# Performance work log

Hardware: AMD Instinct MI355X
Metric: run time of the kernel (lower is better)

The kernel has to match this reference:

```python
import jax, jax.numpy as jnp
import numpy as np

EPS = 1e-8

def _gelu(x):
    return jax.nn.gelu(x, approximate=False)  # torch F.gelu default (erf)

def _film_pool(feat, q, film_w, film_b, hid_w, hid_b, fin_w, fin_b):
    # feat: (B,C,H,W), q: (B,Q,E)
    B, C, H, W = feat.shape
    f = feat.reshape(B, C, H * W).transpose(0, 2, 1)            # (B,HW,C)
    gb = q @ film_w + film_b                                    # (B,Q,2C)
    gamma, beta = jnp.split(gb, 2, axis=-1)                     # (B,Q,C) each
    mod = gamma[:, :, None, :] * f[:, None, :, :] + beta[:, :, None, :]  # (B,Q,HW,C)
    h = _gelu(mod @ hid_w + hid_b)                              # (B,Q,HW,Hh)
    attn = jax.nn.sigmoid(h @ fin_w + fin_b)                    # (B,Q,HW,1)
    pooled = (attn * mod).sum(axis=2) / (attn.sum(axis=2) + EPS)  # (B,Q,C)
    return pooled, attn[..., 0]                                 # attn map (B,Q,HW)

def setup_inputs() -> dict:
    key = jax.random.key(0)
    ks = jax.random.split(key, 32)
    B, Q, E, Hh = 2, 32, 768, 128
    chans = [64, 128, 256]
    hws = [(80, 80), (40, 40), (20, 20)]
    d = {}
    d['feat0'] = jax.random.normal(ks[0], (B, chans[0], *hws[0]), jnp.float32)
    d['feat1'] = jax.random.normal(ks[1], (B, chans[1], *hws[1]), jnp.float32)
    d['feat2'] = jax.random.normal(ks[2], (B, chans[2], *hws[2]), jnp.float32)
    d['fact_embeddings'] = jax.random.normal(ks[3], (B, Q, E), jnp.float32)
    for i, C in enumerate(chans):
        d[f'film_w{i}'] = jax.random.normal(ks[4 + 4 * i], (E, 2 * C), jnp.float32) * 0.02
        d[f'film_b{i}'] = jnp.zeros((2 * C,), jnp.float32)
        d[f'hid_w{i}'] = jax.random.normal(ks[5 + 4 * i], (C, Hh), jnp.float32) * 0.05
        d[f'hid_b{i}'] = jnp.zeros((Hh,), jnp.float32)
        d[f'fin_w{i}'] = jax.random.normal(ks[6 + 4 * i], (Hh, 1), jnp.float32) * 0.05
        d[f'fin_b{i}'] = jnp.zeros((1,), jnp.float32)
    in_dim = sum(chans) + hws[-1][0] * hws[-1][1]  # 448 + 400 = 848
    d['mlp_w1'] = jax.random.normal(ks[20], (in_dim, 512), jnp.float32) * 0.02
    d['mlp_b1'] = jnp.zeros((512,), jnp.float32)
    d['mlp_w2'] = jax.random.normal(ks[21], (512, 256), jnp.float32) * 0.02
    d['mlp_b2'] = jnp.zeros((256,), jnp.float32)
    d['mlp_w3'] = jax.random.normal(ks[22], (256, 1), jnp.float32) * 0.02
    d['mlp_b3'] = jnp.zeros((1,), jnp.float32)
    return d

def reference(feat0, feat1, feat2, fact_embeddings,
              film_w0, film_b0, hid_w0, hid_b0, fin_w0, fin_b0,
              film_w1, film_b1, hid_w1, hid_b1, fin_w1, fin_b1,
              film_w2, film_b2, hid_w2, hid_b2, fin_w2, fin_b2,
              mlp_w1, mlp_b1, mlp_w2, mlp_b2, mlp_w3, mlp_b3):
    q = fact_embeddings
    p0, _ = _film_pool(feat0, q, film_w0, film_b0, hid_w0, hid_b0, fin_w0, fin_b0)
    p1, _ = _film_pool(feat1, q, film_w1, film_b1, hid_w1, hid_b1, fin_w1, fin_b1)
    p2, a2 = _film_pool(feat2, q, film_w2, film_b2, hid_w2, hid_b2, fin_w2, fin_b2)
    cat = jnp.concatenate([p0, p1, p2, a2], axis=2)  # (B,Q,848)
    x = _gelu(cat @ mlp_w1 + mlp_b1)
    x = _gelu(x @ mlp_w2 + mlp_b2)
    logits = (x @ mlp_w3 + mlp_b3)[..., 0]  # (B,Q)
    return logits
```

## Files before the change

kernel.cpp:

```cpp
#include <hip/hip_runtime.h>
#include <math.h>

#define BQ 64
#define HH 128
#define EPS 1e-8f

typedef short bf16x8 __attribute__((ext_vector_type(8)));
typedef float f32x4  __attribute__((ext_vector_type(4)));

__device__ __forceinline__ float gelu_exact(float x) {
    return 0.5f * x * (1.0f + erff(x * 0.70710678118654752440f));
}

__device__ __forceinline__ unsigned bf16_rne(float x) {
    unsigned u = __float_as_uint(x);
    return (u + 0x7FFFu + ((u >> 16) & 1u)) >> 16;
}
__device__ __forceinline__ uint2 split_pack(float a, float b) {
    unsigned ha = bf16_rne(a);
    float fa = __uint_as_float(ha << 16);
    unsigned la = bf16_rne(a - fa);
    unsigned hb = bf16_rne(b);
    float fb = __uint_as_float(hb << 16);
    unsigned lb = bf16_rne(b - fb);
    uint2 r; r.x = ha | (hb << 16); r.y = la | (lb << 16);
    return r;
}

__global__ __launch_bounds__(256)
void film2_kernel(const float* __restrict__ qe,
                  const float* __restrict__ fw0, const float* __restrict__ fb0,
                  const float* __restrict__ fw1, const float* __restrict__ fb1,
                  const float* __restrict__ fw2, const float* __restrict__ fb2,
                  float* __restrict__ gb0, float* __restrict__ gb1, float* __restrict__ gb2)
{
    __shared__ float sq[768];
    __shared__ float sP[256];
    const int tid = threadIdx.x, bq = blockIdx.x, chunk = blockIdx.y;
    int s, o0;
    if (chunk == 0)      { s = 0; o0 = 0; }
    else if (chunk <= 2) { s = 1; o0 = (chunk - 1) * 128; }
    else                 { s = 2; o0 = (chunk - 3) * 128; }
    const float* fw  = s == 0 ? fw0 : s == 1 ? fw1 : fw2;
    const float* fbv = s == 0 ? fb0 : s == 1 ? fb1 : fb2;
    float* gb        = s == 0 ? gb0 : s == 1 ? gb1 : gb2;
    const int twoC = 128 << s;

    for (int i = tid; i < 768; i += 256) sq[i] = qe[bq * 768 + i];
    __syncthreads();

    const int o = o0 + (tid & 127), half = tid >> 7;
    const int e0 = half * 384;
    float a0 = 0.f, a1 = 0.f;
    #pragma unroll 2
    for (int e = 0; e < 384; e += 2) {
        a0 = fmaf(sq[e0 + e],     fw[(e0 + e) * twoC + o],     a0);
        a1 = fmaf(sq[e0 + e + 1], fw[(e0 + e + 1) * twoC + o], a1);
    }
    sP[tid] = a0 + a1;
    __syncthreads();
    if (tid < 128) {
        int oo = o0 + tid;
        gb[bq * twoC + oo] = sP[tid] + sP[tid + 128] + fbv[oo];
    }
}

__global__ __launch_bounds__(256)
void b2_kernel(const float* __restrict__ gb0, const float* __restrict__ gb1,
               const float* __restrict__ gb2,
               const float* __restrict__ hw0_, const float* __restrict__ hb0,
               const float* __restrict__ hw1_, const float* __restrict__ hb1,
               const float* __restrict__ hw2_, const float* __restrict__ hb2,
               float* __restrict__ b20, float* __restrict__ b21, float* __restrict__ b22)
{
    __shared__ float sBeta[256];
    __shared__ float sP[256];
    const int tid = threadIdx.x, bq = blockIdx.x, s = blockIdx.y;
    const float* gb = s == 0 ? gb0 : s == 1 ? gb1 : gb2;
    const float* hw = s == 0 ? hw0_ : s == 1 ? hw1_ : hw2_;
    const float* hb = s == 0 ? hb0 : s == 1 ? hb1 : hb2;
    float* b2       = s == 0 ? b20 : s == 1 ? b21 : b22;
    const int C = 64 << s;

    for (int i = tid; i < C; i += 256) sBeta[i] = gb[bq * 2 * C + C + i];
    __syncthreads();
    const int j = tid & 127, half = tid >> 7;
    const int c0 = half * (C / 2);
    float acc = 0.f;
    for (int c = 0; c < C / 2; ++c)
        acc = fmaf(sBeta[c0 + c], hw[(c0 + c) * HH + j], acc);
    sP[tid] = acc;
    __syncthreads();
    if (tid < 128) b2[bq * HH + tid] = hb[tid] + sP[tid] + sP[tid + 128];
}

__global__ __launch_bounds__(256)
void pack_feat_kernel(const float* __restrict__ f0, const float* __restrict__ f1,
                      const float* __restrict__ f2,
                      unsigned short* __restrict__ p0h, unsigned short* __restrict__ p0l,
                      unsigned short* __restrict__ p1h, unsigned short* __restrict__ p1l,
                      unsigned short* __restrict__ p2h, unsigned short* __restrict__ p2l)
{
    int i = blockIdx.x * 256 + threadIdx.x;
    const float* f; unsigned short *oh, *ol; int HW; int idx;
    if (i < 102400)      { f = f0; oh = p0h; ol = p0l; HW = 6400; idx = i; }
    else if (i < 153600) { f = f1; oh = p1h; ol = p1l; HW = 1600; idx = i - 102400; }
    else if (i < 179200) { f = f2; oh = p2h; ol = p2l; HW = 400;  idx = i - 153600; }
    else return;
    const int px = idx % HW;
    const int cgb = idx / HW;
    const float* src = f + ((size_t)cgb * 8) * HW + px;
    float a[8];
    #pragma unroll
    for (int k = 0; k < 8; ++k) a[k] = src[(size_t)k * HW];
    unsigned hwd[4], lwd[4];
    #pragma unroll
    for (int k = 0; k < 4; ++k) {
        uint2 p = split_pack(a[2 * k], a[2 * k + 1]);
        hwd[k] = p.x; lwd[k] = p.y;
    }
    *(uint4*)&oh[(size_t)idx * 8] = make_uint4(hwd[0], hwd[1], hwd[2], hwd[3]);
    *(uint4*)&ol[(size_t)idx * 8] = make_uint4(lwd[0], lwd[1], lwd[2], lwd[3]);
}

__global__ __launch_bounds__(256)
void pack_gw_kernel(const float* __restrict__ gb0, const float* __restrict__ gb1,
                    const float* __restrict__ gb2,
                    const float* __restrict__ hw0_, const float* __restrict__ hw1_,
                    const float* __restrict__ hw2_,
                    unsigned short* __restrict__ g0h, unsigned short* __restrict__ g0l,
                    unsigned short* __restrict__ g1h, unsigned short* __restrict__ g1l,
                    unsigned short* __restrict__ g2h, unsigned short* __restrict__ g2l)
{
    int i = blockIdx.x * 256 + threadIdx.x;
    const float *gb, *hw; unsigned short *oh, *ol; int C, idx;
    if (i < 65536)       { gb = gb0; hw = hw0_; oh = g0h; ol = g0l; C = 64;  idx = i; }
    else if (i < 196608) { gb = gb1; hw = hw1_; oh = g1h; ol = g1l; C = 128; idx = i - 65536; }
    else if (i < 458752) { gb = gb2; hw = hw2_; oh = g2h; ol = g2l; C = 256; idx = i - 196608; }
    else return;
    const int j  = idx & 127;
    const int cg = (idx >> 7) % (C / 8);
    const int bq = idx / (128 * (C / 8));
    const int c0 = cg * 8;
    const float* g = gb + bq * 2 * C;
    float a[8];
    #pragma unroll
    for (int k = 0; k < 8; ++k) a[k] = g[c0 + k] * hw[(size_t)(c0 + k) * HH + j];
    unsigned hwd[4], lwd[4];
    #pragma unroll
    for (int k = 0; k < 4; ++k) {
        uint2 p = split_pack(a[2 * k], a[2 * k + 1]);
        hwd[k] = p.x; lwd[k] = p.y;
    }
    *(uint4*)&oh[(size_t)idx * 8] = make_uint4(hwd[0], hwd[1], hwd[2], hwd[3]);
    *(uint4*)&ol[(size_t)idx * 8] = make_uint4(lwd[0], lwd[1], lwd[2], lwd[3]);
}

template<int C, bool WRITE_ATTN>
__device__ __forceinline__
void pool_body(const float* __restrict__ feat, int HW,
               const unsigned short* __restrict__ fh, const unsigned short* __restrict__ fl,
               const unsigned short* __restrict__ gwh, const unsigned short* __restrict__ gwl,
               const float* __restrict__ b2, const float* __restrict__ finw,
               const float* __restrict__ finb,
               float* __restrict__ Sout, float* __restrict__ attn_out,
               int bq, int tile,
               unsigned short* sB, float* sAttn)
{
    const int tid  = threadIdx.x;
    const int w    = tid >> 6;
    const int lane = tid & 63;
    const int l15  = lane & 15, l4 = lane >> 4;
    const int b    = bq >> 5;
    const int px0  = tile * 256;
    constexpr int CG = C / 8;
    const float* fbase = feat + (size_t)b * C * HW;

    f32x4 acc[2][8];
    #pragma unroll
    for (int jt = 0; jt < 8; ++jt) {
        float bv = b2[bq * HH + jt * 16 + l15];
        acc[0][jt] = (f32x4){bv, bv, bv, bv};
        acc[1][jt] = (f32x4){bv, bv, bv, bv};
    }

    const int apx0 = min(px0 + (w * 2 + 0) * 16 + l15, HW - 1);
    const int apx1 = min(px0 + (w * 2 + 1) * 16 + l15, HW - 1);
    const unsigned short* fhp = fh + (size_t)b * CG * HW * 8;
    const unsigned short* flp = fl + (size_t)b * CG * HW * 8;
    const unsigned short* gbh = gwh + (size_t)bq * CG * 128 * 8;
    const unsigned short* gbl = gwl + (size_t)bq * CG * 128 * 8;

    for (int ks = 0; ks < CG / 4; ++ks) {
        const size_t arow = (size_t)(ks * 4 + l4) * HW;
        const bf16x8 Ahi0 = *(const bf16x8*)(fhp + (arow + apx0) * 8);
        const bf16x8 Alo0 = *(const bf16x8*)(flp + (arow + apx0) * 8);
        const bf16x8 Ahi1 = *(const bf16x8*)(fhp + (arow + apx1) * 8);
        const bf16x8 Alo1 = *(const bf16x8*)(flp + (arow + apx1) * 8);

        {
            const uint4* srcH = (const uint4*)(gbh + (size_t)ks * 4096);
            const uint4* srcL = (const uint4*)(gbl + (size_t)ks * 4096);
            uint4* dst = (uint4*)sB;
            dst[tid]       = srcH[tid];
            dst[512 + tid] = srcL[tid];
        }
        __syncthreads();

        const int bofs = (l4 * 128 + l15) * 8;
        #pragma unroll
        for (int jt = 0; jt < 8; ++jt) {
            const bf16x8 Bhi = *(const bf16x8*)(sB + bofs + jt * 128);
            const bf16x8 Blo = *(const bf16x8*)(sB + 4096 + bofs + jt * 128);
            acc[0][jt] = __builtin_amdgcn_mfma_f32_16x16x32_bf16(Alo0, Bhi, acc[0][jt], 0, 0, 0);
            acc[0][jt] = __builtin_amdgcn_mfma_f32_16x16x32_bf16(Ahi0, Blo, acc[0][jt], 0, 0, 0);
            acc[0][jt] = __builtin_amdgcn_mfma_f32_16x16x32_bf16(Ahi0, Bhi, acc[0][jt], 0, 0, 0);
            acc[1][jt] = __builtin_amdgcn_mfma_f32_16x16x32_bf16(Alo1, Bhi, acc[1][jt], 0, 0, 0);
            acc[1][jt] = __builtin_amdgcn_mfma_f32_16x16x32_bf16(Ahi1, Blo, acc[1][jt], 0, 0, 0);
            acc[1][jt] = __builtin_amdgcn_mfma_f32_16x16x32_bf16(Ahi1, Bhi, acc[1][jt], 0, 0, 0);
        }
        __syncthreads();
    }

    const float fb0 = finb[0];
    #pragma unroll
    for (int p = 0; p < 2; ++p) {
        float pl[4] = {0.f, 0.f, 0.f, 0.f};
        #pragma unroll
        for (int jt = 0; jt < 8; ++jt) {
            float fw = finw[jt * 16 + l15];
            #pragma unroll
            for (int r = 0; r < 4; ++r)
                pl[r] = fmaf(gelu_exact(acc[p][jt][r]), fw, pl[r]);
        }
        #pragma unroll
        for (int r = 0; r < 4; ++r) {
            pl[r] += __shfl_xor(pl[r], 1);
            pl[r] += __shfl_xor(pl[r], 2);
            pl[r] += __shfl_xor(pl[r], 4);
            pl[r] += __shfl_xor(pl[r], 8);
        }
        if (l15 == 0) {
            #pragma unroll
            for (int r = 0; r < 4; ++r) {
                int lpx = (w * 2 + p) * 16 + l4 * 4 + r;
                int px  = px0 + lpx;
                float a = (px < HW) ? 1.0f / (1.0f + expf(-(pl[r] + fb0))) : 0.0f;
                sAttn[lpx] = a;
                if (WRITE_ATTN && px < HW) attn_out[bq * HW + px] = a;
            }
        }
    }
    __syncthreads();

    if (tid < 256) {
        float sa = sAttn[tid];
        #pragma unroll
        for (int d = 1; d < 64; d <<= 1) sa += __shfl_xor(sa, d);
        if (lane == 0) atomicAdd(&Sout[bq * (C + 1) + C], sa);
    }

    constexpr int CPW = C / 8;
    #pragma unroll 1
    for (int ci = 0; ci < CPW; ++ci) {
        const int c2 = w * CPW + ci;
        const float* fr = fbase + (size_t)c2 * HW;
        float s = 0.f;
        #pragma unroll
        for (int k = 0; k < 4; ++k) {
            int lpx = lane + 64 * k;
            int gc = min(px0 + lpx, HW - 1);
            s = fmaf(fr[gc], sAttn[lpx], s);
        }
        #pragma unroll
        for (int d = 1; d < 64; d <<= 1) s += __shfl_xor(s, d);
        if (lane == 0) atomicAdd(&Sout[bq * (C + 1) + c2], s);
    }
}

__global__ __launch_bounds__(512)
void pool_fused(const float* __restrict__ feat0, const float* __restrict__ feat1,
                const float* __restrict__ feat2,
                const unsigned short* __restrict__ f0h, const unsigned short* __restrict__ f0l,
                const unsigned short* __restrict__ f1h, const unsigned short* __restrict__ f1l,
                const unsigned short* __restrict__ f2h, const unsigned short* __restrict__ f2l,
                const unsigned short* __restrict__ g0h, const unsigned short* __restrict__ g0l,
                const unsigned short* __restrict__ g1h, const unsigned short* __restrict__ g1l,
                const unsigned short* __restrict__ g2h, const unsigned short* __restrict__ g2l,
                const float* __restrict__ b20, const float* __restrict__ b21,
                const float* __restrict__ b22,
                const float* __restrict__ finw0, const float* __restrict__ finb0,
                const float* __restrict__ finw1, const float* __restrict__ finb1,
                const float* __restrict__ finw2, const float* __restrict__ finb2,
                float* __restrict__ S0, float* __restrict__ S1, float* __restrict__ S2,
                float* __restrict__ attn2)
{
    __shared__ __align__(16) unsigned short sB[8192];
    __shared__ float sAttn[256];
    const int blk = blockIdx.x;
    if (blk < 128) {
        int bq = blk >> 1, t = blk & 1;
        pool_body<256, true>(feat2, 400, f2h, f2l, g2h, g2l, b22, finw2, finb2,
                             S2, attn2, bq, t, sB, sAttn);
    } else if (blk < 576) {
        int bb = blk - 128; int bq = bb / 7, t = bb % 7;
        pool_body<128, false>(feat1, 1600, f1h, f1l, g1h, g1l, b21, finw1, finb1,
                              S1, nullptr, bq, t, sB, sAttn);
    } else {
        int bb = blk - 576; int bq = bb / 25, t = bb % 25;
        pool_body<64, false>(feat0, 6400, f0h, f0l, g0h, g0l, b20, finw0, finb0,
                             S0, nullptr, bq, t, sB, sAttn);
    }
}

__global__ __launch_bounds__(256)
void mlp1_kernel(const float* __restrict__ S0, const float* __restrict__ S1,
                 const float* __restrict__ S2,
                 const float* __restrict__ gb0, const float* __restrict__ gb1,
                 const float* __restrict__ gb2,
                 const float* __restrict__ attn2,
                 const float* __restrict__ w1, const float* __restrict__ b1,
                 float* __restrict__ X1)
{
    __shared__ float sCat[848];
    __shared__ float sP[256];
    const int tid = threadIdx.x, bq = blockIdx.x;

    for (int i = tid; i < 448; i += 256) {
        int sc, c;
        if (i < 64)       { sc = 0; c = i; }
        else if (i < 192) { sc = 1; c = i - 64; }
        else              { sc = 2; c = i - 192; }
        const int C = 64 << sc;
        const float* So = (sc == 0) ? S0 : (sc == 1) ? S1 : S2;
        const float* g  = (sc == 0) ? gb0 : (sc == 1) ? gb1 : gb2;
        float Sa = So[bq * (C + 1) + C];
        float Sf = So[bq * (C + 1) + c];
        float gamma = g[bq * 2 * C + c];
        float beta  = g[bq * 2 * C + C + c];
        sCat[i] = (gamma * Sf + beta * Sa) / (Sa + EPS);
    }
    for (int i = tid; i < 400; i += 256) sCat[448 + i] = attn2[bq * 400 + i];
    __syncthreads();

    const int o = blockIdx.y * 128 + (tid & 127), half = tid >> 7;
    const int k0 = half * 424;
    float a0 = 0.f, a1 = 0.f;
    #pragma unroll 2
    for (int k = 0; k < 424; k += 2) {
        a0 = fmaf(sCat[k0 + k],     w1[(k0 + k) * 512 + o],     a0);
        a1 = fmaf(sCat[k0 + k + 1], w1[(k0 + k + 1) * 512 + o], a1);
    }
    sP[tid] = a0 + a1;
    __syncthreads();
    if (tid < 128) {
        int oo = blockIdx.y * 128 + tid;
        X1[bq * 512 + oo] = sP[tid] + sP[tid + 128] + b1[oo];
    }
}

__global__ __launch_bounds__(256)
void mlp23_kernel(const float* __restrict__ X1,
                  const float* __restrict__ w2, const float* __restrict__ b2,
                  const float* __restrict__ w3, const float* __restrict__ b3,
                  float* __restrict__ out)
{
    __shared__ float sX1[512];
    __shared__ float sX2[256];
    __shared__ float sR[4];
    const int tid = threadIdx.x, bq = blockIdx.x;
    for (int i = tid; i < 512; i += 256) sX1[i] = gelu_exact(X1[bq * 512 + i]);
    __syncthreads();
    float a0 = b2[tid], a1 = 0.f, a2 = 0.f, a3 = 0.f;
    #pragma unroll 4
    for (int k = 0; k < 512; k += 4) {
        a0 = fmaf(sX1[k],     w2[(k)     * 256 + tid], a0);
        a1 = fmaf(sX1[k + 1], w2[(k + 1) * 256 + tid], a1);
        a2 = fmaf(sX1[k + 2], w2[(k + 2) * 256 + tid], a2);
        a3 = fmaf(sX1[k + 3], w2[(k + 3) * 256 + tid], a3);
    }
    sX2[tid] = gelu_exact((a0 + a1) + (a2 + a3));
    __syncthreads();
    float p = sX2[tid] * w3[tid];
    #pragma unroll
    for (int d = 1; d < 64; d <<= 1) p += __shfl_xor(p, d);
    if ((tid & 63) == 0) sR[tid >> 6] = p;
    __syncthreads();
    if (tid == 0) out[bq] = sR[0] + sR[1] + sR[2] + sR[3] + b3[0];
}

extern "C" void kernel_launch(void* const* d_in, const int* in_sizes, int n_in,
                              void* d_out, int out_size, void* d_ws, size_t ws_size,
                              hipStream_t stream)
{
    const float* feat0 = (const float*)d_in[0];
    const float* feat1 = (const float*)d_in[1];
    const float* feat2 = (const float*)d_in[2];
    const float* qe    = (const float*)d_in[3];
    const float* film_w0 = (const float*)d_in[4];
    const float* film_b0 = (const float*)d_in[5];
    const float* hid_w0  = (const float*)d_in[6];
    const float* hid_b0  = (const float*)d_in[7];
    const float* fin_w0  = (const float*)d_in[8];
    const float* fin_b0  = (const float*)d_in[9];
    const float* film_w1 = (const float*)d_in[10];
    const float* film_b1 = (const float*)d_in[11];
    const float* hid_w1  = (const float*)d_in[12];
    const float* hid_b1  = (const float*)d_in[13];
    const float* fin_w1  = (const float*)d_in[14];
    const float* fin_b1  = (const float*)d_in[15];
    const float* film_w2 = (const float*)d_in[16];
    const float* film_b2 = (const float*)d_in[17];
    const float* hid_w2  = (const float*)d_in[18];
    const float* hid_b2  = (const float*)d_in[19];
    const float* fin_w2  = (const float*)d_in[20];
    const float* fin_b2  = (const float*)d_in[21];
    const float* mlp_w1  = (const float*)d_in[22];
    const float* mlp_b1  = (const float*)d_in[23];
    const float* mlp_w2  = (const float*)d_in[24];
    const float* mlp_b2  = (const float*)d_in[25];
    const float* mlp_w3  = (const float*)d_in[26];
    const float* mlp_b3  = (const float*)d_in[27];

    float* ws = (float*)d_ws;
    float* S0    = ws;
    float* S1    = ws + 4160;
    float* S2    = ws + 12416;
    float* gb0   = ws + 28864;
    float* gb1   = ws + 37056;
    float* gb2   = ws + 53440;
    float* b20   = ws + 86208;
    float* b21   = ws + 94400;
    float* b22   = ws + 102592;
    float* attn2 = ws + 110784;
    float* X1    = ws + 136384;

    unsigned short* us = (unsigned short*)(ws + 169216);
    unsigned short* f0h = us;
    unsigned short* f0l = f0h + 819200;
    unsigned short* f1h = f0l + 819200;
    unsigned short* f1l = f1h + 409600;
    unsigned short* f2h = f1l + 409600;
    unsigned short* f2l = f2h + 204800;
    unsigned short* g0h = f2l + 204800;
    unsigned short* g0l = g0h + 524288;
    unsigned short* g1h = g0l + 524288;
    unsigned short* g1l = g1h + 1048576;
    unsigned short* g2h = g1l + 1048576;
    unsigned short* g2l = g2h + 2097152;

    hipMemsetAsync(d_ws, 0, 28864 * sizeof(float), stream);

    pack_feat_kernel<<<700, 256, 0, stream>>>(
        feat0, feat1, feat2, f0h, f0l, f1h, f1l, f2h, f2l);

    film2_kernel<<<dim3(BQ, 7), 256, 0, stream>>>(
        qe, film_w0, film_b0, film_w1, film_b1, film_w2, film_b2,
        gb0, gb1, gb2);

    pack_gw_kernel<<<1792, 256, 0, stream>>>(
        gb0, gb1, gb2, hid_w0, hid_w1, hid_w2,
        g0h, g0l, g1h, g1l, g2h, g2l);

    b2_kernel<<<dim3(BQ, 3), 256, 0, stream>>>(
        gb0, gb1, gb2,
        hid_w0, hid_b0, hid_w1, hid_b1, hid_w2, hid_b2,
        b20, b21, b22);

    pool_fused<<<2176, 512, 0, stream>>>(
        feat0, feat1, feat2,
        f0h, f0l, f1h, f1l, f2h, f2l,
        g0h, g0l, g1h, g1l, g2h, g2l,
        b20, b21, b22,
        fin_w0, fin_b0, fin_w1, fin_b1, fin_w2, fin_b2,
        S0, S1, S2, attn2);

    mlp1_kernel<<<dim3(BQ, 4), 256, 0, stream>>>(
        S0, S1, S2, gb0, gb1, gb2, attn2, mlp_w1, mlp_b1, X1);

    mlp23_kernel<<<BQ, 256, 0, stream>>>(
        X1, mlp_w2, mlp_b2, mlp_w3, mlp_b3, (float*)d_out);
}
```

Before: 258.0 us.

## Process two queries per pool block and merge prep kernels into two launches

```diff
diff --git a/kernel.cpp b/kernel.cpp
--- a/kernel.cpp
+++ b/kernel.cpp
@@ -27,81 +27,14 @@
     return r;
 }
 
-__global__ __launch_bounds__(256)
-void film2_kernel(const float* __restrict__ qe,
-                  const float* __restrict__ fw0, const float* __restrict__ fb0,
-                  const float* __restrict__ fw1, const float* __restrict__ fb1,
-                  const float* __restrict__ fw2, const float* __restrict__ fb2,
-                  float* __restrict__ gb0, float* __restrict__ gb1, float* __restrict__ gb2)
-{
-    __shared__ float sq[768];
-    __shared__ float sP[256];
-    const int tid = threadIdx.x, bq = blockIdx.x, chunk = blockIdx.y;
-    int s, o0;
-    if (chunk == 0)      { s = 0; o0 = 0; }
-    else if (chunk <= 2) { s = 1; o0 = (chunk - 1) * 128; }
-    else                 { s = 2; o0 = (chunk - 3) * 128; }
-    const float* fw  = s == 0 ? fw0 : s == 1 ? fw1 : fw2;
-    const float* fbv = s == 0 ? fb0 : s == 1 ? fb1 : fb2;
-    float* gb        = s == 0 ? gb0 : s == 1 ? gb1 : gb2;
-    const int twoC = 128 << s;
-
-    for (int i = tid; i < 768; i += 256) sq[i] = qe[bq * 768 + i];
-    __syncthreads();
-
-    const int o = o0 + (tid & 127), half = tid >> 7;
-    const int e0 = half * 384;
-    float a0 = 0.f, a1 = 0.f;
-    #pragma unroll 2
-    for (int e = 0; e < 384; e += 2) {
-        a0 = fmaf(sq[e0 + e],     fw[(e0 + e) * twoC + o],     a0);
-        a1 = fmaf(sq[e0 + e + 1], fw[(e0 + e + 1) * twoC + o], a1);
-    }
-    sP[tid] = a0 + a1;
-    __syncthreads();
-    if (tid < 128) {
-        int oo = o0 + tid;
-        gb[bq * twoC + oo] = sP[tid] + sP[tid + 128] + fbv[oo];
-    }
-}
-
-__global__ __launch_bounds__(256)
-void b2_kernel(const float* __restrict__ gb0, const float* __restrict__ gb1,
-               const float* __restrict__ gb2,
-               const float* __restrict__ hw0_, const float* __restrict__ hb0,
-               const float* __restrict__ hw1_, const float* __restrict__ hb1,
-               const float* __restrict__ hw2_, const float* __restrict__ hb2,
-               float* __restrict__ b20, float* __restrict__ b21, float* __restrict__ b22)
-{
-    __shared__ float sBeta[256];
-    __shared__ float sP[256];
-    const int tid = threadIdx.x, bq = blockIdx.x, s = blockIdx.y;
-    const float* gb = s == 0 ? gb0 : s == 1 ? gb1 : gb2;
-    const float* hw = s == 0 ? hw0_ : s == 1 ? hw1_ : hw2_;
-    const float* hb = s == 0 ? hb0 : s == 1 ? hb1 : hb2;
-    float* b2       = s == 0 ? b20 : s == 1 ? b21 : b22;
-    const int C = 64 << s;
-
-    for (int i = tid; i < C; i += 256) sBeta[i] = gb[bq * 2 * C + C + i];
-    __syncthreads();
-    const int j = tid & 127, half = tid >> 7;
-    const int c0 = half * (C / 2);
-    float acc = 0.f;
-    for (int c = 0; c < C / 2; ++c)
-        acc = fmaf(sBeta[c0 + c], hw[(c0 + c) * HH + j], acc);
-    sP[tid] = acc;
-    __syncthreads();
-    if (tid < 128) b2[bq * HH + tid] = hb[tid] + sP[tid] + sP[tid + 128];
-}
-
-__global__ __launch_bounds__(256)
-void pack_feat_kernel(const float* __restrict__ f0, const float* __restrict__ f1,
-                      const float* __restrict__ f2,
-                      unsigned short* __restrict__ p0h, unsigned short* __restrict__ p0l,
-                      unsigned short* __restrict__ p1h, unsigned short* __restrict__ p1l,
-                      unsigned short* __restrict__ p2h, unsigned short* __restrict__ p2l)
-{
-    int i = blockIdx.x * 256 + threadIdx.x;
+__device__ __forceinline__
+void pack_feat_body(int i,
+                    const float* __restrict__ f0, const float* __restrict__ f1,
+                    const float* __restrict__ f2,
+                    unsigned short* __restrict__ p0h, unsigned short* __restrict__ p0l,
+                    unsigned short* __restrict__ p1h, unsigned short* __restrict__ p1l,
+                    unsigned short* __restrict__ p2h, unsigned short* __restrict__ p2l)
+{
     const float* f; unsigned short *oh, *ol; int HW; int idx;
     if (i < 102400)      { f = f0; oh = p0h; ol = p0l; HW = 6400; idx = i; }
     else if (i < 153600) { f = f1; oh = p1h; ol = p1l; HW = 1600; idx = i - 102400; }
@@ -124,37 +57,115 @@
 }
 
 __global__ __launch_bounds__(256)
-void pack_gw_kernel(const float* __restrict__ gb0, const float* __restrict__ gb1,
-                    const float* __restrict__ gb2,
-                    const float* __restrict__ hw0_, const float* __restrict__ hw1_,
-                    const float* __restrict__ hw2_,
-                    unsigned short* __restrict__ g0h, unsigned short* __restrict__ g0l,
-                    unsigned short* __restrict__ g1h, unsigned short* __restrict__ g1l,
-                    unsigned short* __restrict__ g2h, unsigned short* __restrict__ g2l)
-{
-    int i = blockIdx.x * 256 + threadIdx.x;
-    const float *gb, *hw; unsigned short *oh, *ol; int C, idx;
-    if (i < 65536)       { gb = gb0; hw = hw0_; oh = g0h; ol = g0l; C = 64;  idx = i; }
-    else if (i < 196608) { gb = gb1; hw = hw1_; oh = g1h; ol = g1l; C = 128; idx = i - 65536; }
-    else if (i < 458752) { gb = gb2; hw = hw2_; oh = g2h; ol = g2l; C = 256; idx = i - 196608; }
-    else return;
-    const int j  = idx & 127;
-    const int cg = (idx >> 7) % (C / 8);
-    const int bq = idx / (128 * (C / 8));
-    const int c0 = cg * 8;
-    const float* g = gb + bq * 2 * C;
-    float a[8];
-    #pragma unroll
-    for (int k = 0; k < 8; ++k) a[k] = g[c0 + k] * hw[(size_t)(c0 + k) * HH + j];
-    unsigned hwd[4], lwd[4];
-    #pragma unroll
-    for (int k = 0; k < 4; ++k) {
-        uint2 p = split_pack(a[2 * k], a[2 * k + 1]);
-        hwd[k] = p.x; lwd[k] = p.y;
-    }
-    *(uint4*)&oh[(size_t)idx * 8] = make_uint4(hwd[0], hwd[1], hwd[2], hwd[3]);
-    *(uint4*)&ol[(size_t)idx * 8] = make_uint4(lwd[0], lwd[1], lwd[2], lwd[3]);
-}
+void prep1_kernel(const float* __restrict__ f0, const float* __restrict__ f1,
+                  const float* __restrict__ f2,
+                  unsigned short* __restrict__ p0h, unsigned short* __restrict__ p0l,
+                  unsigned short* __restrict__ p1h, unsigned short* __restrict__ p1l,
+                  unsigned short* __restrict__ p2h, unsigned short* __restrict__ p2l,
+                  const float* __restrict__ qe,
+                  const float* __restrict__ fw0, const float* __restrict__ fb0,
+                  const float* __restrict__ fw1, const float* __restrict__ fb1,
+                  const float* __restrict__ fw2, const float* __restrict__ fb2,
+                  float* __restrict__ gb0, float* __restrict__ gb1, float* __restrict__ gb2)
+{
+    const int tid = threadIdx.x;
+    if (blockIdx.x < 700) {
+        pack_feat_body(blockIdx.x * 256 + tid, f0, f1, f2, p0h, p0l, p1h, p1l, p2h, p2l);
+        return;
+    }
+    __shared__ float sq[768];
+    __shared__ float sP[256];
+    const int bb = blockIdx.x - 700;
+    const int chunk = bb >> 6, bq = bb & 63;
+    int s, o0;
+    if (chunk == 0)      { s = 0; o0 = 0; }
+    else if (chunk <= 2) { s = 1; o0 = (chunk - 1) * 128; }
+    else                 { s = 2; o0 = (chunk - 3) * 128; }
+    const float* fw  = s == 0 ? fw0 : s == 1 ? fw1 : fw2;
+    const float* fbv = s == 0 ? fb0 : s == 1 ? fb1 : fb2;
+    float* gb        = s == 0 ? gb0 : s == 1 ? gb1 : gb2;
+    const int twoC = 128 << s;
+
+    for (int i = tid; i < 768; i += 256) sq[i] = qe[bq * 768 + i];
+    __syncthreads();
+    const int o = o0 + (tid & 127), half = tid >> 7;
+    const int e0 = half * 384;
+    float a0 = 0.f, a1 = 0.f;
+    #pragma unroll 2
+    for (int e = 0; e < 384; e += 2) {
+        a0 = fmaf(sq[e0 + e],     fw[(e0 + e) * twoC + o],     a0);
+        a1 = fmaf(sq[e0 + e + 1], fw[(e0 + e + 1) * twoC + o], a1);
+    }
+    sP[tid] = a0 + a1;
+    __syncthreads();
+    if (tid < 128) {
+        int oo = o0 + tid;
+        gb[bq * twoC + oo] = sP[tid] + sP[tid + 128] + fbv[oo];
+    }
+}
+
+__global__ __launch_bounds__(256)
+void prep2_kernel(const float* __restrict__ gb0, const float* __restrict__ gb1,
+                  const float* __restrict__ gb2,
+                  const float* __restrict__ hw0_, const float* __restrict__ hb0,
+                  const float* __restrict__ hw1_, const float* __restrict__ hb1,
+                  const float* __restrict__ hw2_, const float* __restrict__ hb2,
+                  unsigned short* __restrict__ g0h, unsigned short* __restrict__ g0l,
+                  unsigned short* __restrict__ g1h, unsigned short* __restrict__ g1l,
+                  unsigned short* __restrict__ g2h, unsigned short* __restrict__ g2l,
+                  float* __restrict__ b20, float* __restrict__ b21, float* __restrict__ b22)
+{
+    const int tid = threadIdx.x;
+    if (blockIdx.x < 1792) {
+        int i = blockIdx.x * 256 + tid;
+        const float *gb, *hw; unsigned short *oh, *ol; int C, idx;
+        if (i < 65536)       { gb = gb0; hw = hw0_; oh = g0h; ol = g0l; C = 64;  idx = i; }
+        else if (i < 196608) { gb = gb1; hw = hw1_; oh = g1h; ol = g1l; C = 128; idx = i - 65536; }
+        else                 { gb = gb2; hw = hw2_; oh = g2h; ol = g2l; C = 256; idx = i - 196608; }
+        const int j  = idx & 127;
+        const int cg = (idx >> 7) % (C / 8);
+        const int bq = idx / (128 * (C / 8));
+        const int c0 = cg * 8;
+        const float* g = gb + bq * 2 * C;
+        float a[8];
+        #pragma unroll
+        for (int k = 0; k < 8; ++k) a[k] = g[c0 + k] * hw[(size_t)(c0 + k) * HH + j];
+        unsigned hwd[4], lwd[4];
+        #pragma unroll
+        for (int k = 0; k < 4; ++k) {
+            uint2 p = split_pack(a[2 * k], a[2 * k + 1]);
+            hwd[k] = p.x; lwd[k] = p.y;
+        }
+        *(uint4*)&oh[(size_t)idx * 8] = make_uint4(hwd[0], hwd[1], hwd[2], hwd[3]);
+        *(uint4*)&ol[(size_t)idx * 8] = make_uint4(lwd[0], lwd[1], lwd[2], lwd[3]);
+        return;
+    }
+    __shared__ float sBeta[256];
+    __shared__ float sP[256];
+    const int bb = blockIdx.x - 1792;
+    const int s = bb >> 6, bq = bb & 63;
+    const float* gb = s == 0 ? gb0 : s == 1 ? gb1 : gb2;
+    const float* hw = s == 0 ? hw0_ : s == 1 ? hw1_ : hw2_;
+    const float* hb = s == 0 ? hb0 : s == 1 ? hb1 : hb2;
+    float* b2       = s == 0 ? b20 : s == 1 ? b21 : b22;
+    const int C = 64 << s;
+
+    for (int i = tid; i < C; i += 256) sBeta[i] = gb[bq * 2 * C + C + i];
+    __syncthreads();
+    const int j = tid & 127, half = tid >> 7;
+    const int c0 = half * (C / 2);
+    float acc = 0.f;
+    for (int c = 0; c < C / 2; ++c)
+        acc = fmaf(sBeta[c0 + c], hw[(c0 + c) * HH + j], acc);
+    sP[tid] = acc;
+    __syncthreads();
+    if (tid < 128) b2[bq * HH + tid] = hb[tid] + sP[tid] + sP[tid + 128];
+}
+
+#define MFMA3(ACC, ALO, AHI, BH, BL)                                            \
+    ACC = __builtin_amdgcn_mfma_f32_16x16x32_bf16(ALO, BH, ACC, 0, 0, 0);       \
+    ACC = __builtin_amdgcn_mfma_f32_16x16x32_bf16(AHI, BL, ACC, 0, 0, 0);       \
+    ACC = __builtin_amdgcn_mfma_f32_16x16x32_bf16(AHI, BH, ACC, 0, 0, 0);
 
 template<int C, bool WRITE_ATTN>
 __device__ __forceinline__
@@ -164,32 +175,38 @@
                const float* __restrict__ b2, const float* __restrict__ finw,
                const float* __restrict__ finb,
                float* __restrict__ Sout, float* __restrict__ attn_out,
-               int bq, int tile,
+               int b, int qp, int tile,
                unsigned short* sB, float* sAttn)
 {
     const int tid  = threadIdx.x;
     const int w    = tid >> 6;
     const int lane = tid & 63;
     const int l15  = lane & 15, l4 = lane >> 4;
-    const int b    = bq >> 5;
     const int px0  = tile * 256;
     constexpr int CG = C / 8;
+    const int bq0 = b * 32 + qp * 2;
+    const int bq1 = bq0 + 1;
     const float* fbase = feat + (size_t)b * C * HW;
 
-    f32x4 acc[2][8];
+    f32x4 accA[2][8], accB[2][8];
     #pragma unroll
     for (int jt = 0; jt < 8; ++jt) {
-        float bv = b2[bq * HH + jt * 16 + l15];
-        acc[0][jt] = (f32x4){bv, bv, bv, bv};
-        acc[1][jt] = (f32x4){bv, bv, bv, bv};
+        float bv0 = b2[bq0 * HH + jt * 16 + l15];
+        float bv1 = b2[bq1 * HH + jt * 16 + l15];
+        accA[0][jt] = (f32x4){bv0, bv0, bv0, bv0};
+        accA[1][jt] = (f32x4){bv0, bv0, bv0, bv0};
+        accB[0][jt] = (f32x4){bv1, bv1, bv1, bv1};
+        accB[1][jt] = (f32x4){bv1, bv1, bv1, bv1};
     }
 
     const int apx0 = min(px0 + (w * 2 + 0) * 16 + l15, HW - 1);
     const int apx1 = min(px0 + (w * 2 + 1) * 16 + l15, HW - 1);
     const unsigned short* fhp = fh + (size_t)b * CG * HW * 8;
     const unsigned short* flp = fl + (size_t)b * CG * HW * 8;
-    const unsigned short* gbh = gwh + (size_t)bq * CG * 128 * 8;
-    const unsigned short* gbl = gwl + (size_t)bq * CG * 128 * 8;
+    const unsigned short* q0h = gwh + (size_t)bq0 * CG * 128 * 8;
+    const unsigned short* q0l = gwl + (size_t)bq0 * CG * 128 * 8;
+    const unsigned short* q1h = gwh + (size_t)bq1 * CG * 128 * 8;
+    const unsigned short* q1l = gwl + (size_t)bq1 * CG * 128 * 8;
 
     for (int ks = 0; ks < CG / 4; ++ks) {
         const size_t arow = (size_t)(ks * 4 + l4) * HW;
@@ -197,67 +214,76 @@
         const bf16x8 Alo0 = *(const bf16x8*)(flp + (arow + apx0) * 8);
         const bf16x8 Ahi1 = *(const bf16x8*)(fhp + (arow + apx1) * 8);
         const bf16x8 Alo1 = *(const bf16x8*)(flp + (arow + apx1) * 8);
-
         {
-            const uint4* srcH = (const uint4*)(gbh + (size_t)ks * 4096);
-            const uint4* srcL = (const uint4*)(gbl + (size_t)ks * 4096);
             uint4* dst = (uint4*)sB;
-            dst[tid]       = srcH[tid];
-            dst[512 + tid] = srcL[tid];
+            dst[tid]        = ((const uint4*)(q0h + (size_t)ks * 4096))[tid];
+            dst[512  + tid] = ((const uint4*)(q0l + (size_t)ks * 4096))[tid];
+            dst[1024 + tid] = ((const uint4*)(q1h + (size_t)ks * 4096))[tid];
+            dst[1536 + tid] = ((const uint4*)(q1l + (size_t)ks * 4096))[tid];
         }
         __syncthreads();
-
         const int bofs = (l4 * 128 + l15) * 8;
         #pragma unroll
         for (int jt = 0; jt < 8; ++jt) {
-            const bf16x8 Bhi = *(const bf16x8*)(sB + bofs + jt * 128);
-            const bf16x8 Blo = *(const bf16x8*)(sB + 4096 + bofs + jt * 128);
-            acc[0][jt] = __builtin_amdgcn_mfma_f32_16x16x32_bf16(Alo0, Bhi, acc[0][jt], 0, 0, 0);
-            acc[0][jt] = __builtin_amdgcn_mfma_f32_16x16x32_bf16(Ahi0, Blo, acc[0][jt], 0, 0, 0);
-            acc[0][jt] = __builtin_amdgcn_mfma_f32_16x16x32_bf16(Ahi0, Bhi, acc[0][jt], 0, 0, 0);
-            acc[1][jt] = __builtin_amdgcn_mfma_f32_16x16x32_bf16(Alo1, Bhi, acc[1][jt], 0, 0, 0);
-            acc[1][jt] = __builtin_amdgcn_mfma_f32_16x16x32_bf16(Ahi1, Blo, acc[1][jt], 0, 0, 0);
-            acc[1][jt] = __builtin_amdgcn_mfma_f32_16x16x32_bf16(Ahi1, Bhi, acc[1][jt], 0, 0, 0);
+            const bf16x8 B0h = *(const bf16x8*)(sB + bofs + jt * 128);
+            const bf16x8 B0l = *(const bf16x8*)(sB + 4096 + bofs + jt * 128);
+            MFMA3(accA[0][jt], Alo0, Ahi0, B0h, B0l)
+            MFMA3(accA[1][jt], Alo1, Ahi1, B0h, B0l)
+            const bf16x8 B1h = *(const bf16x8*)(sB + 8192 + bofs + jt * 128);
+            const bf16x8 B1l = *(const bf16x8*)(sB + 12288 + bofs + jt * 128);
+            MFMA3(accB[0][jt], Alo0, Ahi0, B1h, B1l)
+            MFMA3(accB[1][jt], Alo1, Ahi1, B1h, B1l)
         }
         __syncthreads();
     }
 
     const float fb0 = finb[0];
     #pragma unroll
-    for (int p = 0; p < 2; ++p) {
-        float pl[4] = {0.f, 0.f, 0.f, 0.f};
+    for (int pt = 0; pt < 2; ++pt) {
+        float p0[4] = {0.f, 0.f, 0.f, 0.f};
+        float p1[4] = {0.f, 0.f, 0.f, 0.f};
         #pragma unroll
         for (int jt = 0; jt < 8; ++jt) {
-            float fw = finw[jt * 16 + l15];
+            float fwv = finw[jt * 16 + l15];
             #pragma unroll
-            for (int r = 0; r < 4; ++r)
-                pl[r] = fmaf(gelu_exact(acc[p][jt][r]), fw, pl[r]);
+            for (int r = 0; r < 4; ++r) {
+                p0[r] = fmaf(gelu_exact(accA[pt][jt][r]), fwv, p0[r]);
+                p1[r] = fmaf(gelu_exact(accB[pt][jt][r]), fwv, p1[r]);
+            }
         }
         #pragma unroll
         for (int r = 0; r < 4; ++r) {
-            pl[r] += __shfl_xor(pl[r], 1);
-            pl[r] += __shfl_xor(pl[r], 2);
-            pl[r] += __shfl_xor(pl[r], 4);
-            pl[r] += __shfl_xor(pl[r], 8);
+            p0[r] += __shfl_xor(p0[r], 1);  p1[r] += __shfl_xor(p1[r], 1);
+            p0[r] += __shfl_xor(p0[r], 2);  p1[r] += __shfl_xor(p1[r], 2);
+            p0[r] += __shfl_xor(p0[r], 4);  p1[r] += __shfl_xor(p1[r], 4);
+            p0[r] += __shfl_xor(p0[r], 8);  p1[r] += __shfl_xor(p1[r], 8);
         }
         if (l15 == 0) {
             #pragma unroll
             for (int r = 0; r < 4; ++r) {
-                int lpx = (w * 2 + p) * 16 + l4 * 4 + r;
+                int lpx = (w * 2 + pt) * 16 + l4 * 4 + r;
                 int px  = px0 + lpx;
-                float a = (px < HW) ? 1.0f / (1.0f + expf(-(pl[r] + fb0))) : 0.0f;
-                sAttn[lpx] = a;
-                if (WRITE_ATTN && px < HW) attn_out[bq * HW + px] = a;
+                float a0v = (px < HW) ? 1.0f / (1.0f + expf(-(p0[r] + fb0))) : 0.0f;
+                float a1v = (px < HW) ? 1.0f / (1.0f + expf(-(p1[r] + fb0))) : 0.0f;
+                sAttn[lpx]       = a0v;
+                sAttn[256 + lpx] = a1v;
+                if (WRITE_ATTN && px < HW) {
+                    attn_out[bq0 * HW + px] = a0v;
+                    attn_out[bq1 * HW + px] = a1v;
+                }
             }
         }
     }
     __syncthreads();
 
-    if (tid < 256) {
+    {
         float sa = sAttn[tid];
         #pragma unroll
         for (int d = 1; d < 64; d <<= 1) sa += __shfl_xor(sa, d);
-        if (lane == 0) atomicAdd(&Sout[bq * (C + 1) + C], sa);
+        if (lane == 0) {
+            int bqx = (tid < 256) ? bq0 : bq1;
+            atomicAdd(&Sout[bqx * (C + 1) + C], sa);
+        }
     }
 
     constexpr int CPW = C / 8;
@@ -265,28 +291,36 @@
     for (int ci = 0; ci < CPW; ++ci) {
         const int c2 = w * CPW + ci;
         const float* fr = fbase + (size_t)c2 * HW;
-        float s = 0.f;
+        float s0 = 0.f, s1 = 0.f;
         #pragma unroll
         for (int k = 0; k < 4; ++k) {
             int lpx = lane + 64 * k;
             int gc = min(px0 + lpx, HW - 1);
-            s = fmaf(fr[gc], sAttn[lpx], s);
-        }
-        #pragma unroll
-        for (int d = 1; d < 64; d <<= 1) s += __shfl_xor(s, d);
-        if (lane == 0) atomicAdd(&Sout[bq * (C + 1) + c2], s);
+            float fv = fr[gc];
+            s0 = fmaf(fv, sAttn[lpx], s0);
+            s1 = fmaf(fv, sAttn[256 + lpx], s1);
+        }
+        #pragma unroll
+        for (int d = 1; d < 64; d <<= 1) {
+            s0 += __shfl_xor(s0, d);
+            s1 += __shfl_xor(s1, d);
+        }
+        if (lane == 0) {
+            atomicAdd(&Sout[bq0 * (C + 1) + c2], s0);
+            atomicAdd(&Sout[bq1 * (C + 1) + c2], s1);
+        }
     }
 }
 
 __global__ __launch_bounds__(512)
-void pool_fused(const float* __restrict__ feat0, const float* __restrict__ feat1,
-                const float* __restrict__ feat2,
-                const unsigned short* __restrict__ f0h, const unsigned short* __restrict__ f0l,
+void pool_fused(const unsigned short* __restrict__ f0h, const unsigned short* __restrict__ f0l,
                 const unsigned short* __restrict__ f1h, const unsigned short* __restrict__ f1l,
                 const unsigned short* __restrict__ f2h, const unsigned short* __restrict__ f2l,
                 const unsigned short* __restrict__ g0h, const unsigned short* __restrict__ g0l,
                 const unsigned short* __restrict__ g1h, const unsigned short* __restrict__ g1l,
                 const unsigned short* __restrict__ g2h, const unsigned short* __restrict__ g2l,
+                const float* __restrict__ feat0, const float* __restrict__ feat1,
+                const float* __restrict__ feat2,
                 const float* __restrict__ b20, const float* __restrict__ b21,
                 const float* __restrict__ b22,
                 const float* __restrict__ finw0, const float* __restrict__ finb0,
@@ -295,21 +329,24 @@
                 float* __restrict__ S0, float* __restrict__ S1, float* __restrict__ S2,
                 float* __restrict__ attn2)
 {
-    __shared__ __align__(16) unsigned short sB[8192];
-    __shared__ float sAttn[256];
+    __shared__ __align__(16) unsigned short sB[16384];
+    __shared__ float sAttn[512];
     const int blk = blockIdx.x;
-    if (blk < 128) {
-        int bq = blk >> 1, t = blk & 1;
+    if (blk < 64) {
+        int bt = blk >> 4, qp = blk & 15;
+        int b = bt >> 1, t = bt & 1;
         pool_body<256, true>(feat2, 400, f2h, f2l, g2h, g2l, b22, finw2, finb2,
-                             S2, attn2, bq, t, sB, sAttn);
-    } else if (blk < 576) {
-        int bb = blk - 128; int bq = bb / 7, t = bb % 7;
+                             S2, attn2, b, qp, t, sB, sAttn);
+    } else if (blk < 288) {
+        int bb = blk - 64; int bt = bb >> 4, qp = bb & 15;
+        int b = bt / 7, t = bt % 7;
         pool_body<128, false>(feat1, 1600, f1h, f1l, g1h, g1l, b21, finw1, finb1,
-                              S1, nullptr, bq, t, sB, sAttn);
+                              S1, nullptr, b, qp, t, sB, sAttn);
     } else {
-        int bb = blk - 576; int bq = bb / 25, t = bb % 25;
+        int bb = blk - 288; int bt = bb >> 4, qp = bb & 15;
+        int b = bt / 25, t = bt % 25;
         pool_body<64, false>(feat0, 6400, f0h, f0l, g0h, g0l, b20, finw0, finb0,
-                             S0, nullptr, bq, t, sB, sAttn);
+                             S0, nullptr, b, qp, t, sB, sAttn);
     }
 }
 
@@ -451,26 +488,21 @@
 
     hipMemsetAsync(d_ws, 0, 28864 * sizeof(float), stream);
 
-    pack_feat_kernel<<<700, 256, 0, stream>>>(
-        feat0, feat1, feat2, f0h, f0l, f1h, f1l, f2h, f2l);
-
-    film2_kernel<<<dim3(BQ, 7), 256, 0, stream>>>(
+    prep1_kernel<<<1148, 256, 0, stream>>>(
+        feat0, feat1, feat2, f0h, f0l, f1h, f1l, f2h, f2l,
         qe, film_w0, film_b0, film_w1, film_b1, film_w2, film_b2,
         gb0, gb1, gb2);
 
-    pack_gw_kernel<<<1792, 256, 0, stream>>>(
-        gb0, gb1, gb2, hid_w0, hid_w1, hid_w2,
-        g0h, g0l, g1h, g1l, g2h, g2l);
-
-    b2_kernel<<<dim3(BQ, 3), 256, 0, stream>>>(
+    prep2_kernel<<<1984, 256, 0, stream>>>(
         gb0, gb1, gb2,
         hid_w0, hid_b0, hid_w1, hid_b1, hid_w2, hid_b2,
+        g0h, g0l, g1h, g1l, g2h, g2l,
         b20, b21, b22);
 
-    pool_fused<<<2176, 512, 0, stream>>>(
-        feat0, feat1, feat2,
+    pool_fused<<<1088, 512, 0, stream>>>(
         f0h, f0l, f1h, f1l, f2h, f2l,
         g0h, g0l, g1h, g1l, g2h, g2l,
+        feat0, feat1, feat2,
         b20, b21, b22,
         fin_w0, fin_b0, fin_w1, fin_b1, fin_w2, fin_b2,
         S0, S1, S2, attn2);
```

Result: faster. 233.8 us (-9.4%).
